# Optimization experiments

Hardware: AMD Instinct MI355X
Metric: run time of the kernel (lower is better)

The kernel has to match this reference:

```python
import jax, jax.numpy as jnp
import numpy as np

AN = 1.0      # bandwidth a_n
SIGMA = 1.0   # Gaussian kernel scale
_EPS = 1e-32


def setup_inputs() -> dict:
    key = jax.random.key(0)
    k1, k2, k3 = jax.random.split(key, 3)
    n = 8192
    log_h = jax.random.normal(k1, (n, 1), dtype=jnp.float32)
    durations = jax.random.uniform(k2, (n,), dtype=jnp.float32)
    events = jax.random.randint(k3, (n,), 0, 2, dtype=jnp.int32)
    return {"log_h": log_h, "durations": durations, "events": events}


def reference(log_h, durations, events):
    theta = log_h.reshape(-1)                         # (n,)
    n = theta.shape[0]
    # residuals e = -(theta - log(Y)); note original adds 1e-32 before log
    e = -(theta - jnp.log(durations + _EPS))          # (n,)
    perm = jnp.argsort(e)                             # sort order of e
    e_sorted = e[perm]                                # (n,) ascending
    # Original code sorts [indices, dur, ev, theta] by the indices column,
    # which reorders the side arrays by the INVERSE permutation.
    inv = jnp.argsort(perm)
    ev = events.astype(jnp.float32)[inv]              # (n,)
    th = theta[inv]                                   # (n,)

    diff = (e_sorted[:, None] - e_sorted[None, :]) / AN   # (n, n)
    # Normal(0, SIGMA) log pdf at diff
    log_pdf = -0.5 * (diff / SIGMA) ** 2 - jnp.log(SIGMA * jnp.sqrt(2.0 * jnp.pi))
    # cond_E_i = sum_j pdf_ij * ev_j / (n*an) + eps-per-element
    cond_E = jnp.sum(jnp.exp(log_pdf) * ev / (n * AN) + _EPS, axis=1)   # (n,)
    # Normal(0, SIGMA) cdf at diff
    cdf = 0.5 * (1.0 + jax.lax.erf(diff / (SIGMA * jnp.sqrt(2.0))))
    surv = jnp.sum(cdf / n, axis=1)                   # (n,)

    loss = -jnp.sum((jnp.log(cond_E) - jnp.log(surv) + th) * ev / n)
    return loss
```

## Files before the change

kernel.cpp:

```cpp
#include <hip/hip_runtime.h>
#include <math.h>
#include <stdint.h>

#define RB 256
#define JT 512
#define GM 2048
#define YS 64

#define SCALE 0.84932180028801904f
#define SQRT2PI 2.5066282746310002f
#define KFP 0.46971863934f
#define LN2 0.69314718056f

__device__ __forceinline__ uint64_t order_key(float f, int idx) {
  unsigned u = __float_as_uint(f);
  u = (u & 0x80000000u) ? ~u : (u | 0x80000000u);
  return ((uint64_t)u << 32) | (unsigned)idx;
}

__device__ __forceinline__ float e_of(const float* theta, const float* dur, int i) {
  return logf(dur[i] + 1e-32f) - theta[i];
}

__device__ __forceinline__ void grid_geom(const float* xs, int n, float* x0, float* hx) {
  float a = xs[0] - 7.0f;
  float b = xs[n - 1] + 7.0f;
  *x0 = a;
  *hx = (b - a) / (float)(GM - 1);
}

__global__ __launch_bounds__(RB) void rank_part_kernel(
    const float* __restrict__ theta, const float* __restrict__ dur,
    int* __restrict__ rank_part, int n) {
  __shared__ uint64_t kt[JT];
  const int i = blockIdx.x * RB + threadIdx.x;
  uint64_t ki = order_key(e_of(theta, dur, i), i);
  const int jbase = blockIdx.y * JT;
  for (int t = threadIdx.x; t < JT; t += RB) {
    int j = jbase + t;
    kt[t] = order_key(e_of(theta, dur, j), j);
  }
  __syncthreads();
  int cnt = 0;
  #pragma unroll 8
  for (int jj = 0; jj < JT; ++jj) cnt += (kt[jj] < ki) ? 1 : 0;
  rank_part[blockIdx.y * n + i] = cnt;
}

__global__ __launch_bounds__(RB) void scatter_kernel(
    const float* __restrict__ theta, const float* __restrict__ dur,
    const int* __restrict__ ev, const int* __restrict__ rank_part,
    float* __restrict__ xs, float* __restrict__ evs, float* __restrict__ th_s,
    float* __restrict__ gbuf, float* __restrict__ out, int n) {
  int k = blockIdx.x * RB + threadIdx.x;
  int r = 0;
  const int nj = n / JT;
  #pragma unroll 16
  for (int jch = 0; jch < nj; ++jch) r += rank_part[jch * n + k];
  xs[r] = SCALE * e_of(theta, dur, k);
  evs[k] = (float)ev[r];
  th_s[k] = theta[r];
  if (k < 4 * GM) gbuf[k] = 0.0f;
  if (k == 0) out[0] = 0.0f;
}

__global__ __launch_bounds__(RB) void gt_kernel(
    const float* __restrict__ xs, const float* __restrict__ evs,
    float* __restrict__ gbuf, int n) {
  float x0, hx;
  grid_geom(xs, n, &x0, &hx);
  int m = blockIdx.x * RB + threadIdx.x;
  float xm = fmaf((float)m, hx, x0);
  const int chunk = n / YS;
  int jb = blockIdx.y * chunk;
  const float P2S = 0.39169197f;
  float a = 0.0f, b = 0.0f, f = 0.0f, d = 0.0f;
  #pragma unroll 8
  for (int jj = 0; jj < chunk; ++jj) {
    float xj = xs[jb + jj];
    float ev = evs[jb + jj];
    float dp = xm - xj;
    float g = __builtin_amdgcn_exp2f(-(dp * dp));
    float evg = ev * g;
    a += g;
    b += evg;
    d = fmaf(dp, evg, d);
    float tt = __builtin_amdgcn_rcpf(fmaf(P2S, __builtin_fabsf(dp), 1.0f));
    float poly = tt * (0.3480242f + tt * (-0.0958798f + tt * 0.7478556f));
    f += __builtin_copysignf(fmaf(-poly, g, 1.0f), dp);
  }
  atomicAdd(&gbuf[m], a);
  atomicAdd(&gbuf[GM + m], b);
  atomicAdd(&gbuf[2 * GM + m], 0.5f * (float)chunk + 0.5f * f);
  atomicAdd(&gbuf[3 * GM + m], d);
}

__global__ __launch_bounds__(RB) void final_kernel(
    const float* __restrict__ xs, const float* __restrict__ evs,
    const float* __restrict__ th_s, const float* __restrict__ gbuf,
    float* __restrict__ out, int n) {
  float x0, hx;
  grid_geom(xs, n, &x0, &hx);
  const float* A = gbuf;
  const float* B = gbuf + GM;
  const float* F = gbuf + 2 * GM;
  const float* D = gbuf + 3 * GM;
  int i = blockIdx.x * RB + threadIdx.x;

  float term = 0.0f;
  if (i < n) {
    float x = xs[i];
    double u = ((double)x - (double)x0) / (double)hx;
    int m = (int)u;
    m = min(max(m, 0), GM - 2);
    float t = (float)(u - (double)m);
    float t2 = t * t, t3 = t2 * t;
    float h00 = 2.0f * t3 - 3.0f * t2 + 1.0f;
    float h01 = 3.0f * t2 - 2.0f * t3;
    float h10 = t3 - 2.0f * t2 + t;
    float h11 = t3 - t2;
    float Fi = F[m] * h00 + F[m + 1] * h01 +
               hx * KFP * (A[m] * h10 + A[m + 1] * h11);
    float Bi = B[m] * h00 + B[m + 1] * h01 -
               2.0f * LN2 * hx * (D[m] * h10 + D[m + 1] * h11);
    const float fn = (float)n;
    float condE = fmaxf(Bi, 0.0f) * (1.0f / SQRT2PI) / fn + fn * 1e-32f;
    float surv = fmaxf(Fi, 0.25f) / fn;
    term = (__logf(condE) - __logf(surv) + th_s[i]) * evs[i];
  }

  #pragma unroll
  for (int off = 32; off > 0; off >>= 1) term += __shfl_down(term, off, 64);
  __shared__ float red[RB / 64];
  int wave = threadIdx.x >> 6, lane = threadIdx.x & 63;
  if (lane == 0) red[wave] = term;
  __syncthreads();
  if (threadIdx.x == 0) {
    float s = 0.0f;
    #pragma unroll
    for (int w = 0; w < RB / 64; ++w) s += red[w];
    atomicAdd(out, -s / (float)n);
  }
}

extern "C" void kernel_launch(void* const* d_in, const int* in_sizes, int n_in,
                              void* d_out, int out_size, void* d_ws, size_t ws_size,
                              hipStream_t stream) {
  const float* theta = (const float*)d_in[0];
  const float* dur   = (const float*)d_in[1];
  const int*   ev    = (const int*)d_in[2];
  float* out = (float*)d_out;
  const int n = in_sizes[1];

  char* ws = (char*)d_ws;
  int*   rank_part = (int*)ws;   ws += (n / JT) * n * sizeof(int);
  float* xs   = (float*)ws;      ws += n * sizeof(float);
  float* evs  = (float*)ws;      ws += n * sizeof(float);
  float* th_s = (float*)ws;      ws += n * sizeof(float);
  float* gbuf = (float*)ws;      ws += 4 * GM * sizeof(float);

  rank_part_kernel<<<dim3(n / RB, n / JT), RB, 0, stream>>>(theta, dur, rank_part, n);
  scatter_kernel<<<n / RB, RB, 0, stream>>>(theta, dur, ev, rank_part,
                                            xs, evs, th_s, gbuf, out, n);
  gt_kernel<<<dim3(GM / RB, YS), RB, 0, stream>>>(xs, evs, gbuf, n);
  final_kernel<<<n / RB, RB, 0, stream>>>(xs, evs, th_s, gbuf, out, n);
}
```

Measured before the change: 81.53 us.

## Halve interpolation grid, interleave sorted x and events, use float math in final

Halves the Gaussian/CDF interpolation grid (GM 2048→1024) and doubles the j-split (YS 64→128), so the grid-evaluation kernel does half the total work at the same block count. The sorted residuals and event flags are packed into one float2 array so each inner-loop iteration issues a single 8-byte load instead of two. The final kernel replaces double-precision grid indexing with a float reciprocal multiply plus a clamp on t. The coarser grid and float indexing may reduce interpolation accuracy.

```diff
diff --git a/kernel.cpp b/kernel.cpp
--- a/kernel.cpp
+++ b/kernel.cpp
@@ -4,8 +4,8 @@
 
 #define RB 256
 #define JT 512
-#define GM 2048
-#define YS 64
+#define GM 1024
+#define YS 128
 
 #define SCALE 0.84932180028801904f
 #define SQRT2PI 2.5066282746310002f
@@ -22,9 +22,9 @@
   return logf(dur[i] + 1e-32f) - theta[i];
 }
 
-__device__ __forceinline__ void grid_geom(const float* xs, int n, float* x0, float* hx) {
-  float a = xs[0] - 7.0f;
-  float b = xs[n - 1] + 7.0f;
+__device__ __forceinline__ void grid_geom(const float2* xe, int n, float* x0, float* hx) {
+  float a = xe[0].x - 7.0f;
+  float b = xe[n - 1].x + 7.0f;
   *x0 = a;
   *hx = (b - a) / (float)(GM - 1);
 }
@@ -50,25 +50,24 @@
 __global__ __launch_bounds__(RB) void scatter_kernel(
     const float* __restrict__ theta, const float* __restrict__ dur,
     const int* __restrict__ ev, const int* __restrict__ rank_part,
-    float* __restrict__ xs, float* __restrict__ evs, float* __restrict__ th_s,
+    float2* __restrict__ xe, float* __restrict__ th_s,
     float* __restrict__ gbuf, float* __restrict__ out, int n) {
   int k = blockIdx.x * RB + threadIdx.x;
   int r = 0;
   const int nj = n / JT;
   #pragma unroll 16
   for (int jch = 0; jch < nj; ++jch) r += rank_part[jch * n + k];
-  xs[r] = SCALE * e_of(theta, dur, k);
-  evs[k] = (float)ev[r];
+  ((float*)&xe[r])[0] = SCALE * e_of(theta, dur, k);
+  ((float*)&xe[k])[1] = (float)ev[r];
   th_s[k] = theta[r];
   if (k < 4 * GM) gbuf[k] = 0.0f;
   if (k == 0) out[0] = 0.0f;
 }
 
 __global__ __launch_bounds__(RB) void gt_kernel(
-    const float* __restrict__ xs, const float* __restrict__ evs,
-    float* __restrict__ gbuf, int n) {
+    const float2* __restrict__ xe, float* __restrict__ gbuf, int n) {
   float x0, hx;
-  grid_geom(xs, n, &x0, &hx);
+  grid_geom(xe, n, &x0, &hx);
   int m = blockIdx.x * RB + threadIdx.x;
   float xm = fmaf((float)m, hx, x0);
   const int chunk = n / YS;
@@ -77,11 +76,10 @@
   float a = 0.0f, b = 0.0f, f = 0.0f, d = 0.0f;
   #pragma unroll 8
   for (int jj = 0; jj < chunk; ++jj) {
-    float xj = xs[jb + jj];
-    float ev = evs[jb + jj];
-    float dp = xm - xj;
+    float2 q = xe[jb + jj];
+    float dp = xm - q.x;
     float g = __builtin_amdgcn_exp2f(-(dp * dp));
-    float evg = ev * g;
+    float evg = q.y * g;
     a += g;
     b += evg;
     d = fmaf(dp, evg, d);
@@ -96,11 +94,10 @@
 }
 
 __global__ __launch_bounds__(RB) void final_kernel(
-    const float* __restrict__ xs, const float* __restrict__ evs,
-    const float* __restrict__ th_s, const float* __restrict__ gbuf,
-    float* __restrict__ out, int n) {
+    const float2* __restrict__ xe, const float* __restrict__ th_s,
+    const float* __restrict__ gbuf, float* __restrict__ out, int n) {
   float x0, hx;
-  grid_geom(xs, n, &x0, &hx);
+  grid_geom(xe, n, &x0, &hx);
   const float* A = gbuf;
   const float* B = gbuf + GM;
   const float* F = gbuf + 2 * GM;
@@ -109,11 +106,12 @@
 
   float term = 0.0f;
   if (i < n) {
-    float x = xs[i];
-    double u = ((double)x - (double)x0) / (double)hx;
+    float2 q = xe[i];
+    float u = (q.x - x0) * __builtin_amdgcn_rcpf(hx);
     int m = (int)u;
     m = min(max(m, 0), GM - 2);
-    float t = (float)(u - (double)m);
+    float t = u - (float)m;
+    t = fminf(fmaxf(t, 0.0f), 1.0f);
     float t2 = t * t, t3 = t2 * t;
     float h00 = 2.0f * t3 - 3.0f * t2 + 1.0f;
     float h01 = 3.0f * t2 - 2.0f * t3;
@@ -126,7 +124,7 @@
     const float fn = (float)n;
     float condE = fmaxf(Bi, 0.0f) * (1.0f / SQRT2PI) / fn + fn * 1e-32f;
     float surv = fmaxf(Fi, 0.25f) / fn;
-    term = (__logf(condE) - __logf(surv) + th_s[i]) * evs[i];
+    term = (__logf(condE) - __logf(surv) + th_s[i]) * q.y;
   }
 
   #pragma unroll
@@ -153,15 +151,14 @@
   const int n = in_sizes[1];
 
   char* ws = (char*)d_ws;
-  int*   rank_part = (int*)ws;   ws += (n / JT) * n * sizeof(int);
-  float* xs   = (float*)ws;      ws += n * sizeof(float);
-  float* evs  = (float*)ws;      ws += n * sizeof(float);
-  float* th_s = (float*)ws;      ws += n * sizeof(float);
-  float* gbuf = (float*)ws;      ws += 4 * GM * sizeof(float);
+  float2* xe        = (float2*)ws;  ws += n * sizeof(float2);
+  int*    rank_part = (int*)ws;     ws += (n / JT) * n * sizeof(int);
+  float*  th_s      = (float*)ws;   ws += n * sizeof(float);
+  float*  gbuf      = (float*)ws;   ws += 4 * GM * sizeof(float);
 
   rank_part_kernel<<<dim3(n / RB, n / JT), RB, 0, stream>>>(theta, dur, rank_part, n);
   scatter_kernel<<<n / RB, RB, 0, stream>>>(theta, dur, ev, rank_part,
-                                            xs, evs, th_s, gbuf, out, n);
-  gt_kernel<<<dim3(GM / RB, YS), RB, 0, stream>>>(xs, evs, gbuf, n);
-  final_kernel<<<n / RB, RB, 0, stream>>>(xs, evs, th_s, gbuf, out, n);
+                                            xe, th_s, gbuf, out, n);
+  gt_kernel<<<dim3(GM / RB, YS), RB, 0, stream>>>(xe, gbuf, n);
+  final_kernel<<<n / RB, RB, 0, stream>>>(xe, th_s, gbuf, out, n);
 }
```

After: 78.01 us (median of 2 runs). -4.3%, faster.
